# Optimization experiments

Hardware: AMD Instinct MI355X
Metric: run time of the kernel (lower is better)

## Reference

```python
import jax, jax.numpy as jnp
import numpy as np

N = 100_000      # nodes
E = 3_200_000    # directed edges (avg degree 32)
F_IN = 503
C = 32           # GATConv out_channels, heads=1
NEG_SLOPE = 0.2  # PyG GATConv default


def setup_inputs() -> dict:
    key = jax.random.key(0)
    ks = jax.random.split(key, 14)
    x = jax.random.normal(ks[0], (N, F_IN), jnp.float32)
    edge_index = jax.random.randint(ks[1], (2, E), 0, N)
    edge_weight = jax.random.uniform(ks[2], (E, 1), jnp.float32)
    input_mask = jnp.ones((N, 1), jnp.float32)
    # GATConv params (heads=1)
    W_src = jax.random.normal(ks[3], (C, F_IN), jnp.float32) * 0.02
    att_src = jax.random.normal(ks[4], (C,), jnp.float32) * 0.1
    att_dst = jax.random.normal(ks[5], (C,), jnp.float32) * 0.1
    att_edge = jax.random.normal(ks[6], (C,), jnp.float32) * 0.1
    W_edge = jax.random.normal(ks[7], (C, 1), jnp.float32) * 0.1
    bias_conv = jnp.zeros((C,), jnp.float32)
    # dense heads
    Wb = jax.random.normal(ks[8], (1, C), jnp.float32) * 0.1
    bb = jnp.zeros((1,), jnp.float32)
    Ww = jax.random.normal(ks[9], (1, C), jnp.float32) * 0.1
    bw = jnp.zeros((1,), jnp.float32)
    return {"x": x, "edge_index": edge_index, "edge_weight": edge_weight,
            "input_mask": input_mask, "W_src": W_src, "att_src": att_src,
            "att_dst": att_dst, "att_edge": att_edge, "W_edge": W_edge,
            "bias_conv": bias_conv, "Wb": Wb, "bb": bb, "Ww": Ww, "bw": bw}


def reference(x, edge_index, edge_weight, input_mask, W_src, att_src, att_dst,
              att_edge, W_edge, bias_conv, Wb, bb, Ww, bw):
    n = x.shape[0]
    xl = x @ W_src.T                       # [N, C] transformed node features
    a_src = xl @ att_src                   # [N] per-node source attention logit
    a_dst = xl @ att_dst                   # [N]
    src, dst = edge_index[0], edge_index[1]
    # add_self_loops=True with fill_value='mean' for edge_attr (PyG default)
    loop = jnp.arange(n)
    mean_attr = jnp.mean(edge_weight, axis=0, keepdims=True)      # [1,1]
    ea = jnp.concatenate([edge_weight, jnp.broadcast_to(mean_attr, (n, 1))], 0)
    s = jnp.concatenate([src, loop])       # [E+N]
    d = jnp.concatenate([dst, loop])
    a_edge = (ea @ W_edge.T) @ att_edge    # [E+N]
    alpha = jax.nn.leaky_relu(a_src[s] + a_dst[d] + a_edge, NEG_SLOPE)
    # softmax over incoming edges of each destination node
    amax = jax.ops.segment_max(alpha, d, num_segments=n)
    ex = jnp.exp(alpha - amax[d])
    denom = jax.ops.segment_sum(ex, d, num_segments=n)
    w = ex / denom[d]                      # [E+N] attention coeffs
    msg = xl[s] * w[:, None]               # [E+N, C]
    out = jax.ops.segment_sum(msg, d, num_segments=n) + bias_conv  # [N, C]
    h = jax.nn.relu(out)
    biases = (h @ Wb.T + bb) * input_mask  # [N, 1]
    weights = ((h[src] + h[dst]) * 0.5) @ Ww.T + bw  # [E, 1]
    return weights, biases
```

## Files before the change

### kernel.cpp

```cpp
#include <hip/hip_runtime.h>
#include <stdint.h>

#define NN 100000
#define NE 3200000
#define FIN 503
#define COUT 32
#define NSLOPE 0.2f

#define BSH 6
#define NB 1563
#define HB 256
#define EPB (NE / HB)
#define MAXBE 2560
#define NREG (MAXBE / 256)

typedef __bf16 bf16x8 __attribute__((ext_vector_type(8)));
typedef float  f32x4  __attribute__((ext_vector_type(4)));

__device__ __forceinline__ unsigned short bf1(float f) {
    unsigned u = __float_as_uint(f);
    u = (u + 0x7FFFu + ((u >> 16) & 1u)) >> 16;
    return (unsigned short)u;
}
__device__ __forceinline__ unsigned bf2(float a, float b) {
    return (unsigned)bf1(a) | ((unsigned)bf1(b) << 16);
}
__device__ __forceinline__ float unbf(unsigned short h) {
    return __uint_as_float(((unsigned)h) << 16);
}

__global__ __launch_bounds__(256)
void k_stats(const float* __restrict__ ew, float* __restrict__ partial,
             const float* __restrict__ W, uint4* __restrict__ wfrag)
{
    const int t = threadIdx.x;
    const int gid = blockIdx.x * 256 + t;

    if (gid < 2048) {
        int c = gid & 31;
        int quad = (gid >> 5) & 3;
        int chunk = gid >> 7;
        int kb = chunk * 32 + quad * 8;
        float v[8];
        #pragma unroll
        for (int j = 0; j < 8; ++j) {
            int k = kb + j;
            v[j] = (k < FIN) ? W[c * FIN + k] : 0.f;
        }
        uint4 o;
        o.x = bf2(v[0], v[1]); o.y = bf2(v[2], v[3]);
        o.z = bf2(v[4], v[5]); o.w = bf2(v[6], v[7]);
        wfrag[gid] = o;
    }

    const float4* ew4 = (const float4*)ew;
    float s = 0.f;
    for (int i = gid; i < NE / 4; i += gridDim.x * 256) {
        float4 v = ew4[i];
        s += v.x + v.y + v.z + v.w;
    }
    #pragma unroll
    for (int off = 32; off > 0; off >>= 1) s += __shfl_xor(s, off);
    __shared__ float wsum[4];
    if ((t & 63) == 0) wsum[t >> 6] = s;
    __syncthreads();
    if (t == 0) partial[blockIdx.x] = wsum[0] + wsum[1] + wsum[2] + wsum[3];
}

#define GR 64

__global__ __launch_bounds__(256)
void k_gemm(const float* __restrict__ x, const uint4* __restrict__ wfrag,
            const float* __restrict__ att_s, const float* __restrict__ att_d,
            unsigned short* __restrict__ xlb,
            float* __restrict__ a_src, float* __restrict__ a_dst)
{
    __shared__ __align__(16) float xs[GR][36];
    __shared__ __align__(16) unsigned short os[GR * 40];
    const int t = threadIdx.x;
    const int wv = t >> 6, lane = t & 63;
    const int m16 = lane & 15, quad = lane >> 4;
    const int row0 = blockIdx.x * GR;
    const int srow = t >> 5;
    const int scol = t & 31;

    f32x4 acc0 = {0.f, 0.f, 0.f, 0.f};
    f32x4 acc1 = {0.f, 0.f, 0.f, 0.f};
    const int rowf = wv * 16 + m16;

    for (int ch = 0; ch < 16; ++ch) {
        const int k = ch * 32 + scol;
        #pragma unroll
        for (int p = 0; p < 8; ++p) {
            int r = p * 8 + srow;
            int rg = row0 + r;
            rg = (rg < NN) ? rg : (NN - 1);
            xs[r][scol] = (k < FIN) ? x[(size_t)rg * FIN + k] : 0.f;
        }
        __syncthreads();
        float av[8];
        *(f32x4*)&av[0] = *(const f32x4*)&xs[rowf][quad * 8];
        *(f32x4*)&av[4] = *(const f32x4*)&xs[rowf][quad * 8 + 4];
        bf16x8 af;
        #pragma unroll
        for (int j = 0; j < 8; ++j) af[j] = (__bf16)av[j];
        uint4 b0 = wfrag[ch * 128 + quad * 32 + m16];
        uint4 b1 = wfrag[ch * 128 + quad * 32 + 16 + m16];
        acc0 = __builtin_amdgcn_mfma_f32_16x16x32_bf16(af, *(bf16x8*)&b0, acc0, 0, 0, 0);
        acc1 = __builtin_amdgcn_mfma_f32_16x16x32_bf16(af, *(bf16x8*)&b1, acc1, 0, 0, 0);
        __syncthreads();
    }

    #pragma unroll
    for (int r = 0; r < 4; ++r) {
        int rr = wv * 16 + quad * 4 + r;
        os[rr * 40 + m16]      = bf1(acc0[r]);
        os[rr * 40 + 16 + m16] = bf1(acc1[r]);
    }
    __syncthreads();
    {
        int r = t >> 2, c0 = (t & 3) * 8;
        int grow = row0 + r;
        uint4 o = *(const uint4*)&os[r * 40 + c0];
        float s = 0.f, dd = 0.f;
        const unsigned short* oh = (const unsigned short*)&o;
        #pragma unroll
        for (int j = 0; j < 8; ++j) {
            float v = unbf(oh[j]);
            s  += v * att_s[c0 + j];
            dd += v * att_d[c0 + j];
        }
        s  += __shfl_xor(s, 1, 4);  s  += __shfl_xor(s, 2, 4);
        dd += __shfl_xor(dd, 1, 4); dd += __shfl_xor(dd, 2, 4);
        if (grow < NN) {
            *(uint4*)&xlb[(size_t)grow * COUT + c0] = o;
            if ((t & 3) == 0) { a_src[grow] = s; a_dst[grow] = dd; }
        }
    }
}

__global__ __launch_bounds__(512)
void k_hist(const int* __restrict__ ei_dst, unsigned* __restrict__ part)
{
    __shared__ unsigned h[NB];
    for (int i = threadIdx.x; i < NB; i += 512) h[i] = 0u;
    __syncthreads();
    const int base = blockIdx.x * EPB;
    for (int i = threadIdx.x; i < EPB; i += 512)
        atomicAdd(&h[ei_dst[base + i] >> BSH], 1u);
    __syncthreads();
    for (int i = threadIdx.x; i < NB; i += 512)
        part[(size_t)blockIdx.x * NB + i] = h[i];
}

__global__ void k_colscan(unsigned* __restrict__ part, unsigned* __restrict__ colsum)
{
    __shared__ unsigned sm[HB];
    const int t = threadIdx.x;
    const int bkt = blockIdx.x;
    unsigned v = part[(size_t)t * NB + bkt];
    sm[t] = v;
    for (int off = 1; off < HB; off <<= 1) {
        __syncthreads();
        unsigned tv = (t >= off) ? sm[t - off] : 0u;
        __syncthreads();
        sm[t] += tv;
    }
    __syncthreads();
    part[(size_t)t * NB + bkt] = sm[t] - v;
    if (t == HB - 1) colsum[bkt] = sm[t];
}

__global__ void k_bscan(const unsigned* __restrict__ colsum, unsigned* __restrict__ bbase,
                        const float* __restrict__ partial, const float* __restrict__ W_edge,
                        const float* __restrict__ att_e, float* __restrict__ stats)
{
    const int t = threadIdx.x;
    {
        __shared__ float fs[256];
        float ps = partial[t] + partial[t + 256] + partial[t + 512] + partial[t + 768];
        fs[t] = ps;
        __syncthreads();
        for (int off = 128; off > 0; off >>= 1) {
            if (t < off) fs[t] += fs[t + off];
            __syncthreads();
        }
        if (t == 0) {
            stats[0] = fs[0];
            float k = 0.f;
            for (int c = 0; c < COUT; ++c) k += W_edge[c] * att_e[c];
            stats[1] = k;
        }
    }
    __syncthreads();

    __shared__ unsigned sm[256];
    __shared__ unsigned carry;
    if (t == 0) carry = 0u;
    __syncthreads();
    for (int c0 = 0; c0 < NB; c0 += 256) {
        int i = c0 + t;
        unsigned v = (i < NB) ? colsum[i] : 0u;
        sm[t] = v;
        for (int off = 1; off < 256; off <<= 1) {
            __syncthreads();
            unsigned tv = (t >= off) ? sm[t - off] : 0u;
            __syncthreads();
            sm[t] += tv;
        }
        __syncthreads();
        if (i < NB) bbase[i] = carry + sm[t] - v;
        __syncthreads();
        if (t == 0) carry += sm[255];
        __syncthreads();
    }
    if (t == 0) bbase[NB] = carry;
}

__global__ __launch_bounds__(512)
void k_scatter(const int* __restrict__ ei, const float* __restrict__ ew,
               const float* __restrict__ a_src, const float* __restrict__ stats,
               const unsigned* __restrict__ part, const unsigned* __restrict__ bbase,
               uint2* __restrict__ csr)
{
    __shared__ unsigned cur[NB];
    const int b = blockIdx.x;
    for (int i = threadIdx.x; i < NB; i += 512)
        cur[i] = bbase[i] + part[(size_t)b * NB + i];
    __syncthreads();
    const float kc = stats[1];
    const int base = b * EPB;
    for (int i = threadIdx.x; i < EPB; i += 512) {
        int e = base + i;
        int s = ei[e];
        int d = ei[NE + e];
        float pre = a_src[s] + kc * ew[e];
        unsigned pos = atomicAdd(&cur[d >> BSH], 1u);
        csr[pos] = make_uint2((unsigned)s | ((unsigned)(d & 63) << 20),
                              __float_as_uint(pre));
    }
}

__global__ __launch_bounds__(256)
void k_aggr(const uint2* __restrict__ csr, const unsigned* __restrict__ bbase,
            const float* __restrict__ a_src, const float* __restrict__ a_dst,
            const unsigned short* __restrict__ xlb, const float* __restrict__ stats,
            const float* __restrict__ bias_conv, const float* __restrict__ Wb,
            const float* __restrict__ bb, const float* __restrict__ Ww,
            const float* __restrict__ mask, float* __restrict__ out_b,
            float* __restrict__ hw)
{
    __shared__ uint2 rec[MAXBE];
    __shared__ unsigned seg[65], cur[64];
    const int t = threadIdx.x;
    const int b = blockIdx.x;
    const int jb = (int)bbase[b];
    int ne = (int)bbase[b + 1] - jb;
    if (ne > MAXBE) ne = MAXBE;

    uint2 rg[NREG];
    #pragma unroll
    for (int j = 0; j < NREG; ++j) {
        int i = t + j * 256;
        rg[j] = (i < ne) ? csr[jb + i] : make_uint2(0u, 0u);
    }
    if (t < 64) cur[t] = 0u;
    __syncthreads();
    #pragma unroll
    for (int j = 0; j < NREG; ++j)
        if (t + j * 256 < ne) atomicAdd(&cur[rg[j].x >> 20], 1u);
    __syncthreads();
    if (t < 64) {
        unsigned v = cur[t];
        unsigned s = v;
        #pragma unroll
        for (int off = 1; off < 64; off <<= 1) {
            unsigned u = __shfl_up(s, off, 64);
            if (t >= off) s += u;
        }
        seg[t + 1] = s;
        cur[t] = s - v;
        if (t == 0) seg[0] = 0u;
    }
    __syncthreads();
    #pragma unroll
    for (int j = 0; j < NREG; ++j)
        if (t + j * 256 < ne) {
            unsigned pos = atomicAdd(&cur[rg[j].x >> 20], 1u);
            rec[pos] = rg[j];
        }
    __syncthreads();

    const float kmean = stats[1] * (stats[0] * (1.f / NE));
    const int lane = t & 31;
    for (int dl = t >> 5; dl < 64; dl += 8) {
        int d = (b << BSH) + dl;
        if (d >= NN) continue;
        const float adv = a_dst[d];
        float a0 = a_src[d] + adv + kmean;
        a0 = (a0 > 0.f) ? a0 : NSLOPE * a0;
        const float ps = __expf(a0);
        float l = 0.f;
        float acc = ps * unbf(xlb[(size_t)d * COUT + lane]);
        const int j0 = (int)seg[dl], j1 = (int)seg[dl + 1];
        for (int tb = j0; tb < j1; tb += 32) {
            int j = tb + lane;
            float p = 0.f;
            if (j < j1) {
                uint2 en = rec[j];
                float a = __uint_as_float(en.y) + adv;
                a = (a > 0.f) ? a : NSLOPE * a;
                p = __expf(a);
                rec[j].y = __float_as_uint(p);
            }
            l += p;
            int cnte = min(32, j1 - tb);
            #pragma unroll 4
            for (int k = 0; k < cnte; ++k) {
                uint2 en = rec[tb + k];
                acc += __uint_as_float(en.y) *
                       unbf(xlb[(size_t)(en.x & 0xFFFFFu) * COUT + lane]);
            }
        }
        #pragma unroll
        for (int off = 16; off > 0; off >>= 1) l += __shfl_xor(l, off, 32);
        l += ps;
        float h = fmaxf(acc / l + bias_conv[lane], 0.f);
        float pb = h * Wb[lane];
        float pw = h * Ww[lane];
        #pragma unroll
        for (int off = 16; off > 0; off >>= 1) {
            pb += __shfl_xor(pb, off, 32);
            pw += __shfl_xor(pw, off, 32);
        }
        if (lane == 0) {
            out_b[d] = (pb + bb[0]) * mask[d];
            hw[d] = pw;
        }
    }
}

__global__ void k_weights(const int* __restrict__ ei, const float* __restrict__ hw,
                          const float* __restrict__ bw, float* __restrict__ out_w)
{
    int e = blockIdx.x * 256 + threadIdx.x;
    if (e < NE) {
        int s = ei[e], d = ei[NE + e];
        out_w[e] = 0.5f * (hw[s] + hw[d]) + bw[0];
    }
}

extern "C" void kernel_launch(void* const* d_in, const int* in_sizes, int n_in,
                              void* d_out, int out_size, void* d_ws, size_t ws_size,
                              hipStream_t stream)
{
    const float* x        = (const float*)d_in[0];
    const int*   ei       = (const int*)d_in[1];
    const float* ew       = (const float*)d_in[2];
    const float* mask     = (const float*)d_in[3];
    const float* W_src    = (const float*)d_in[4];
    const float* att_src  = (const float*)d_in[5];
    const float* att_dst  = (const float*)d_in[6];
    const float* att_edge = (const float*)d_in[7];
    const float* W_edge   = (const float*)d_in[8];
    const float* bias_c   = (const float*)d_in[9];
    const float* Wb       = (const float*)d_in[10];
    const float* bb       = (const float*)d_in[11];
    const float* Ww       = (const float*)d_in[12];
    const float* bw       = (const float*)d_in[13];
    (void)in_sizes; (void)n_in; (void)out_size; (void)ws_size;

    char* wsp = (char*)d_ws;
    size_t off = 0;
    auto alloc = [&](size_t bytes) -> void* {
        void* p = wsp + off;
        off = (off + bytes + 255) & ~(size_t)255;
        return p;
    };
    unsigned short* xlb    = (unsigned short*)alloc((size_t)NN * COUT * 2);
    uint4*    wfrag  = (uint4*)alloc(2048 * 16);
    float*    a_src  = (float*)alloc((size_t)NN * 4);
    float*    a_dst  = (float*)alloc((size_t)NN * 4);
    float*    stats  = (float*)alloc(256);
    float*    partial= (float*)alloc(1024 * 4);
    unsigned* part   = (unsigned*)alloc((size_t)HB * NB * 4);
    unsigned* colsum = (unsigned*)alloc((size_t)NB * 4);
    unsigned* bbase  = (unsigned*)alloc((size_t)(NB + 1) * 4);
    uint2*    csr    = (uint2*)alloc((size_t)NE * 8);
    float*    hw     = (float*)alloc((size_t)NN * 4);

    float* out_w = (float*)d_out;
    float* out_b = out_w + NE;

    k_stats   <<<1024, 256, 0, stream>>>(ew, partial, W_src, wfrag);
    k_gemm    <<<(NN + GR - 1) / GR, 256, 0, stream>>>(x, wfrag, att_src, att_dst,
                                                       xlb, a_src, a_dst);
    k_hist    <<<HB, 512, 0, stream>>>(ei + NE, part);
    k_colscan <<<NB, HB, 0, stream>>>(part, colsum);
    k_bscan   <<<1, 256, 0, stream>>>(colsum, bbase, partial, W_edge, att_edge, stats);
    k_scatter <<<HB, 512, 0, stream>>>(ei, ew, a_src, stats, part, bbase, csr);
    k_aggr    <<<NB, 256, 0, stream>>>(csr, bbase, a_src, a_dst, xlb, stats,
                                       bias_c, Wb, bb, Ww, mask, out_b, hw);
    k_weights <<<NE / 256, 256, 0, stream>>>(ei, hw, bw, out_w);
}
```

Measured before the change: 530.9 us.

## Fuse preprocessing and scan kernels, double-buffer GEMM staging, vectorize edge weights

Merges the edge-weight sum, weight fragment packing and destination histogram into one kernel. The column scan and bucket scan are folded into a single kernel where the last block to finish runs the global scan, tracked by an atomic counter. Each run thus needs fewer kernel launches and global round trips. The GEMM staging now double-buffers the x tiles in shared memory, which removes one barrier per chunk. The scatter and aggregation kernels move to more blocks with 256 threads and drop register prefetch of CSR records. The weights kernel processes four edges per thread with vector loads and stores.

```diff
diff --git a/kernel.cpp b/kernel.cpp
--- a/kernel.cpp
+++ b/kernel.cpp
@@ -9,10 +9,9 @@
 
 #define BSH 6
 #define NB 1563
-#define HB 256
+#define HB 512
 #define EPB (NE / HB)
 #define MAXBE 2560
-#define NREG (MAXBE / 256)
 
 typedef __bf16 bf16x8 __attribute__((ext_vector_type(8)));
 typedef float  f32x4  __attribute__((ext_vector_type(4)));
@@ -30,11 +29,19 @@
 }
 
 __global__ __launch_bounds__(256)
-void k_stats(const float* __restrict__ ew, float* __restrict__ partial,
-             const float* __restrict__ W, uint4* __restrict__ wfrag)
-{
+void k_pre(const int* __restrict__ ei_dst, const float* __restrict__ ew,
+           const float* __restrict__ W, uint4* __restrict__ wfrag,
+           float* __restrict__ partial, unsigned* __restrict__ part,
+           unsigned* __restrict__ done)
+{
+    __shared__ unsigned h[NB];
+    __shared__ float wsum[4];
     const int t = threadIdx.x;
-    const int gid = blockIdx.x * 256 + t;
+    const int b = blockIdx.x;
+    const int gid = b * 256 + t;
+
+    if (gid == 0) *done = 0u;
+    for (int i = t; i < NB; i += 256) h[i] = 0u;
 
     if (gid < 2048) {
         int c = gid & 31;
@@ -52,19 +59,25 @@
         o.z = bf2(v[4], v[5]); o.w = bf2(v[6], v[7]);
         wfrag[gid] = o;
     }
+    __syncthreads();
+
+    const int base = b * EPB;
+    for (int i = t; i < EPB; i += 256)
+        atomicAdd(&h[ei_dst[base + i] >> BSH], 1u);
 
     const float4* ew4 = (const float4*)ew;
     float s = 0.f;
-    for (int i = gid; i < NE / 4; i += gridDim.x * 256) {
+    for (int i = gid; i < NE / 4; i += HB * 256) {
         float4 v = ew4[i];
         s += v.x + v.y + v.z + v.w;
     }
     #pragma unroll
     for (int off = 32; off > 0; off >>= 1) s += __shfl_xor(s, off);
-    __shared__ float wsum[4];
     if ((t & 63) == 0) wsum[t >> 6] = s;
     __syncthreads();
-    if (t == 0) partial[blockIdx.x] = wsum[0] + wsum[1] + wsum[2] + wsum[3];
+    if (t == 0) partial[b] = wsum[0] + wsum[1] + wsum[2] + wsum[3];
+    for (int i = t; i < NB; i += 256)
+        part[(size_t)b * NB + i] = h[i];
 }
 
 #define GR 64
@@ -75,32 +88,38 @@
             unsigned short* __restrict__ xlb,
             float* __restrict__ a_src, float* __restrict__ a_dst)
 {
-    __shared__ __align__(16) float xs[GR][36];
-    __shared__ __align__(16) unsigned short os[GR * 40];
+    __shared__ __align__(16) float xs[2][GR][36];
+    unsigned short* os = (unsigned short*)&xs[0][0][0];
     const int t = threadIdx.x;
     const int wv = t >> 6, lane = t & 63;
     const int m16 = lane & 15, quad = lane >> 4;
     const int row0 = blockIdx.x * GR;
     const int srow = t >> 5;
     const int scol = t & 31;
-
-    f32x4 acc0 = {0.f, 0.f, 0.f, 0.f};
-    f32x4 acc1 = {0.f, 0.f, 0.f, 0.f};
     const int rowf = wv * 16 + m16;
 
-    for (int ch = 0; ch < 16; ++ch) {
+    auto stage = [&](int ch, int buf) {
         const int k = ch * 32 + scol;
+        const bool ok = (k < FIN);
         #pragma unroll
         for (int p = 0; p < 8; ++p) {
             int r = p * 8 + srow;
             int rg = row0 + r;
             rg = (rg < NN) ? rg : (NN - 1);
-            xs[r][scol] = (k < FIN) ? x[(size_t)rg * FIN + k] : 0.f;
-        }
-        __syncthreads();
+            xs[buf][r][scol] = ok ? x[(size_t)rg * FIN + k] : 0.f;
+        }
+    };
+
+    f32x4 acc0 = {0.f, 0.f, 0.f, 0.f};
+    f32x4 acc1 = {0.f, 0.f, 0.f, 0.f};
+
+    stage(0, 0);
+    for (int ch = 0; ch < 16; ++ch) {
+        __syncthreads();
+        if (ch < 15) stage(ch + 1, (ch + 1) & 1);
         float av[8];
-        *(f32x4*)&av[0] = *(const f32x4*)&xs[rowf][quad * 8];
-        *(f32x4*)&av[4] = *(const f32x4*)&xs[rowf][quad * 8 + 4];
+        *(f32x4*)&av[0] = *(const f32x4*)&xs[ch & 1][rowf][quad * 8];
+        *(f32x4*)&av[4] = *(const f32x4*)&xs[ch & 1][rowf][quad * 8 + 4];
         bf16x8 af;
         #pragma unroll
         for (int j = 0; j < 8; ++j) af[j] = (__bf16)av[j];
@@ -108,7 +127,6 @@
         uint4 b1 = wfrag[ch * 128 + quad * 32 + 16 + m16];
         acc0 = __builtin_amdgcn_mfma_f32_16x16x32_bf16(af, *(bf16x8*)&b0, acc0, 0, 0, 0);
         acc1 = __builtin_amdgcn_mfma_f32_16x16x32_bf16(af, *(bf16x8*)&b1, acc1, 0, 0, 0);
-        __syncthreads();
     }
 
     #pragma unroll
@@ -139,46 +157,42 @@
     }
 }
 
-__global__ __launch_bounds__(512)
-void k_hist(const int* __restrict__ ei_dst, unsigned* __restrict__ part)
-{
-    __shared__ unsigned h[NB];
-    for (int i = threadIdx.x; i < NB; i += 512) h[i] = 0u;
-    __syncthreads();
-    const int base = blockIdx.x * EPB;
-    for (int i = threadIdx.x; i < EPB; i += 512)
-        atomicAdd(&h[ei_dst[base + i] >> BSH], 1u);
-    __syncthreads();
-    for (int i = threadIdx.x; i < NB; i += 512)
-        part[(size_t)blockIdx.x * NB + i] = h[i];
-}
-
-__global__ void k_colscan(unsigned* __restrict__ part, unsigned* __restrict__ colsum)
-{
-    __shared__ unsigned sm[HB];
+__global__ void k_scan(unsigned* __restrict__ part, unsigned* __restrict__ colsum,
+                       unsigned* __restrict__ done, const float* __restrict__ partial,
+                       const float* __restrict__ W_edge, const float* __restrict__ att_e,
+                       float* __restrict__ stats, unsigned* __restrict__ bbase)
+{
+    __shared__ unsigned sm[256];
+    __shared__ unsigned winner;
+    __shared__ unsigned carry;
+    __shared__ float fs[256];
     const int t = threadIdx.x;
     const int bkt = blockIdx.x;
-    unsigned v = part[(size_t)t * NB + bkt];
+
+    unsigned e0 = part[(size_t)(2 * t) * NB + bkt];
+    unsigned e1 = part[(size_t)(2 * t + 1) * NB + bkt];
+    unsigned v = e0 + e1;
     sm[t] = v;
-    for (int off = 1; off < HB; off <<= 1) {
+    for (int off = 1; off < 256; off <<= 1) {
         __syncthreads();
         unsigned tv = (t >= off) ? sm[t - off] : 0u;
         __syncthreads();
         sm[t] += tv;
     }
     __syncthreads();
-    part[(size_t)t * NB + bkt] = sm[t] - v;
-    if (t == HB - 1) colsum[bkt] = sm[t];
-}
-
-__global__ void k_bscan(const unsigned* __restrict__ colsum, unsigned* __restrict__ bbase,
-                        const float* __restrict__ partial, const float* __restrict__ W_edge,
-                        const float* __restrict__ att_e, float* __restrict__ stats)
-{
-    const int t = threadIdx.x;
+    unsigned run = sm[t] - v;
+    part[(size_t)(2 * t) * NB + bkt]     = run;
+    part[(size_t)(2 * t + 1) * NB + bkt] = run + e0;
+    if (t == 255) colsum[bkt] = sm[255];
+
+    __threadfence();
+    __syncthreads();
+    if (t == 0) winner = atomicAdd(done, 1u);
+    __syncthreads();
+    if (winner != NB - 1) return;
+
     {
-        __shared__ float fs[256];
-        float ps = partial[t] + partial[t + 256] + partial[t + 512] + partial[t + 768];
+        float ps = partial[t] + partial[t + 256];
         fs[t] = ps;
         __syncthreads();
         for (int off = 128; off > 0; off >>= 1) {
@@ -193,15 +207,12 @@
         }
     }
     __syncthreads();
-
-    __shared__ unsigned sm[256];
-    __shared__ unsigned carry;
     if (t == 0) carry = 0u;
     __syncthreads();
     for (int c0 = 0; c0 < NB; c0 += 256) {
         int i = c0 + t;
-        unsigned v = (i < NB) ? colsum[i] : 0u;
-        sm[t] = v;
+        unsigned cv = (i < NB) ? atomicAdd(&colsum[i], 0u) : 0u;
+        sm[t] = cv;
         for (int off = 1; off < 256; off <<= 1) {
             __syncthreads();
             unsigned tv = (t >= off) ? sm[t - off] : 0u;
@@ -209,7 +220,7 @@
             sm[t] += tv;
         }
         __syncthreads();
-        if (i < NB) bbase[i] = carry + sm[t] - v;
+        if (i < NB) bbase[i] = carry + sm[t] - cv;
         __syncthreads();
         if (t == 0) carry += sm[255];
         __syncthreads();
@@ -217,7 +228,7 @@
     if (t == 0) bbase[NB] = carry;
 }
 
-__global__ __launch_bounds__(512)
+__global__ __launch_bounds__(256)
 void k_scatter(const int* __restrict__ ei, const float* __restrict__ ew,
                const float* __restrict__ a_src, const float* __restrict__ stats,
                const unsigned* __restrict__ part, const unsigned* __restrict__ bbase,
@@ -225,12 +236,13 @@
 {
     __shared__ unsigned cur[NB];
     const int b = blockIdx.x;
-    for (int i = threadIdx.x; i < NB; i += 512)
+    const int t = threadIdx.x;
+    for (int i = t; i < NB; i += 256)
         cur[i] = bbase[i] + part[(size_t)b * NB + i];
     __syncthreads();
     const float kc = stats[1];
     const int base = b * EPB;
-    for (int i = threadIdx.x; i < EPB; i += 512) {
+    for (int i = t; i < EPB; i += 256) {
         int e = base + i;
         int s = ei[e];
         int d = ei[NE + e];
@@ -258,17 +270,10 @@
     int ne = (int)bbase[b + 1] - jb;
     if (ne > MAXBE) ne = MAXBE;
 
-    uint2 rg[NREG];
-    #pragma unroll
-    for (int j = 0; j < NREG; ++j) {
-        int i = t + j * 256;
-        rg[j] = (i < ne) ? csr[jb + i] : make_uint2(0u, 0u);
-    }
     if (t < 64) cur[t] = 0u;
     __syncthreads();
-    #pragma unroll
-    for (int j = 0; j < NREG; ++j)
-        if (t + j * 256 < ne) atomicAdd(&cur[rg[j].x >> 20], 1u);
+    for (int i = t; i < ne; i += 256)
+        atomicAdd(&cur[csr[jb + i].x >> 20], 1u);
     __syncthreads();
     if (t < 64) {
         unsigned v = cur[t];
@@ -283,12 +288,11 @@
         if (t == 0) seg[0] = 0u;
     }
     __syncthreads();
-    #pragma unroll
-    for (int j = 0; j < NREG; ++j)
-        if (t + j * 256 < ne) {
-            unsigned pos = atomicAdd(&cur[rg[j].x >> 20], 1u);
-            rec[pos] = rg[j];
-        }
+    for (int i = t; i < ne; i += 256) {
+        uint2 r = csr[jb + i];
+        unsigned pos = atomicAdd(&cur[r.x >> 20], 1u);
+        rec[pos] = r;
+    }
     __syncthreads();
 
     const float kmean = stats[1] * (stats[0] * (1.f / NE));
@@ -343,10 +347,17 @@
 __global__ void k_weights(const int* __restrict__ ei, const float* __restrict__ hw,
                           const float* __restrict__ bw, float* __restrict__ out_w)
 {
-    int e = blockIdx.x * 256 + threadIdx.x;
-    if (e < NE) {
-        int s = ei[e], d = ei[NE + e];
-        out_w[e] = 0.5f * (hw[s] + hw[d]) + bw[0];
+    int e4 = blockIdx.x * 256 + threadIdx.x;
+    if (e4 < NE / 4) {
+        int4 s4 = ((const int4*)ei)[e4];
+        int4 d4 = ((const int4*)(ei + NE))[e4];
+        float bwv = bw[0];
+        float4 o;
+        o.x = 0.5f * (hw[s4.x] + hw[d4.x]) + bwv;
+        o.y = 0.5f * (hw[s4.y] + hw[d4.y]) + bwv;
+        o.z = 0.5f * (hw[s4.z] + hw[d4.z]) + bwv;
+        o.w = 0.5f * (hw[s4.w] + hw[d4.w]) + bwv;
+        ((float4*)out_w)[e4] = o;
     }
 }
 
@@ -382,24 +393,24 @@
     float*    a_src  = (float*)alloc((size_t)NN * 4);
     float*    a_dst  = (float*)alloc((size_t)NN * 4);
     float*    stats  = (float*)alloc(256);
-    float*    partial= (float*)alloc(1024 * 4);
+    float*    partial= (float*)alloc((size_t)HB * 4);
     unsigned* part   = (unsigned*)alloc((size_t)HB * NB * 4);
     unsigned* colsum = (unsigned*)alloc((size_t)NB * 4);
     unsigned* bbase  = (unsigned*)alloc((size_t)(NB + 1) * 4);
+    unsigned* done   = (unsigned*)alloc(256);
     uint2*    csr    = (uint2*)alloc((size_t)NE * 8);
     float*    hw     = (float*)alloc((size_t)NN * 4);
 
     float* out_w = (float*)d_out;
     float* out_b = out_w + NE;
 
-    k_stats   <<<1024, 256, 0, stream>>>(ew, partial, W_src, wfrag);
+    k_pre     <<<HB, 256, 0, stream>>>(ei + NE, ew, W_src, wfrag, partial, part, done);
     k_gemm    <<<(NN + GR - 1) / GR, 256, 0, stream>>>(x, wfrag, att_src, att_dst,
                                                        xlb, a_src, a_dst);
-    k_hist    <<<HB, 512, 0, stream>>>(ei + NE, part);
-    k_colscan <<<NB, HB, 0, stream>>>(part, colsum);
-    k_bscan   <<<1, 256, 0, stream>>>(colsum, bbase, partial, W_edge, att_edge, stats);
-    k_scatter <<<HB, 512, 0, stream>>>(ei, ew, a_src, stats, part, bbase, csr);
+    k_scan    <<<NB, 256, 0, stream>>>(part, colsum, done, partial, W_edge,
+                                       att_edge, stats, bbase);
+    k_scatter <<<HB, 256, 0, stream>>>(ei, ew, a_src, stats, part, bbase, csr);
     k_aggr    <<<NB, 256, 0, stream>>>(csr, bbase, a_src, a_dst, xlb, stats,
                                        bias_c, Wb, bb, Ww, mask, out_b, hw);
-    k_weights <<<NE / 256, 256, 0, stream>>>(ei, hw, bw, out_w);
-}
+    k_weights <<<NE / 4 / 256, 256, 0, stream>>>(ei, hw, bw, out_w);
+}
```

Measured after the change: 769.1 us. 1.45x slower.
